# Kernel tuning notes

Hardware: AMD Instinct MI355X
Metric: run time of the kernel (lower is better)

The kernel has to match this reference:

```python
import jax, jax.numpy as jnp
import numpy as np

N_NODES = 50000
N_EDGES = 800000
IN_F = 256
HEADS = 4
C = 32  # out_features // heads = 128 // 4
OUT_F = HEADS * C
NEG_SLOPE = 0.2
BN_EPS = 1e-5


def setup_inputs() -> dict:
    key = jax.random.key(0)
    ks = jax.random.split(key, 6)
    x = jax.random.normal(ks[0], (N_NODES, IN_F), dtype=jnp.float32)
    edge_index = jax.random.randint(ks[1], (2, N_EDGES), 0, N_NODES, dtype=jnp.int64)
    W = jax.random.normal(ks[2], (IN_F, OUT_F), dtype=jnp.float32) * 0.05
    att_src = jax.random.normal(ks[3], (HEADS, C), dtype=jnp.float32) * 0.05
    att_dst = jax.random.normal(ks[4], (HEADS, C), dtype=jnp.float32) * 0.05
    bias = jnp.zeros((OUT_F,), dtype=jnp.float32)
    gamma = jnp.ones((OUT_F,), dtype=jnp.float32)
    beta = jnp.zeros((OUT_F,), dtype=jnp.float32)
    return {"x": x, "edge_index": edge_index, "W": W, "att_src": att_src,
            "att_dst": att_dst, "bias": bias, "gamma": gamma, "beta": beta}


def reference(x, edge_index, W, att_src, att_dst, bias, gamma, beta):
    N = x.shape[0]
    # PyG GATConv adds self-loops by default
    loops = jnp.arange(N, dtype=edge_index.dtype)
    src = jnp.concatenate([edge_index[0], loops])  # [E+N]
    dst = jnp.concatenate([edge_index[1], loops])  # [E+N]

    h = (x @ W).reshape(N, HEADS, C)               # [N, H, C]
    a_src = jnp.sum(h * att_src, axis=-1)          # [N, H]
    a_dst = jnp.sum(h * att_dst, axis=-1)          # [N, H]

    e = a_src[src] + a_dst[dst]                    # [E', H]
    e = jax.nn.leaky_relu(e, NEG_SLOPE)
    # segment softmax over destination neighborhoods (self-loops ensure no empty segments)
    e_max = jax.ops.segment_max(e, dst, num_segments=N)
    e = jnp.exp(e - e_max[dst])
    denom = jax.ops.segment_sum(e, dst, num_segments=N)
    alpha = e / (denom[dst] + 1e-16)               # [E', H]

    msg = h[src] * alpha[:, :, None]               # [E', H, C]
    out = jax.ops.segment_sum(msg, dst, num_segments=N).reshape(N, OUT_F) + bias

    # BatchNorm1d in training mode (batch statistics, biased variance)
    mean = jnp.mean(out, axis=0)
    var = jnp.var(out, axis=0)
    out = (out - mean) * jax.lax.rsqrt(var + BN_EPS) * gamma + beta
    # ELU; dropout is identity in eval / deterministic reference
    return jax.nn.elu(out)
```

## Files before the change

kernel.cpp:

```cpp
#include <hip/hip_runtime.h>
#include <hip/hip_fp16.h>
#include <math.h>

#define NN 50000
#define EE 800000
#define EP (EE + NN)
#define INF_ 256
#define OF 128
#define NEG_SLOPE 0.2f
#define BN_EPS 1e-5f
#define NB 196
#define NWIN 8
#define DPW 6250
#define NCH 32
#define QPC 6250

typedef _Float16 half8 __attribute__((ext_vector_type(8)));
typedef float floatx4 __attribute__((ext_vector_type(4)));
typedef int intx4 __attribute__((ext_vector_type(4)));

__device__ __forceinline__ float lrelu_exp(float v) {
    v = v > 0.f ? v : NEG_SLOPE * v;
    return expf(v);
}

__global__ __launch_bounds__(256) void k_wprep(const float* __restrict__ W, _Float16* __restrict__ wfrag,
                                               float* __restrict__ fsum)
{
    int idx = blockIdx.x * 256 + threadIdx.x;
    if (idx < 256) fsum[idx] = 0.f;
    int j   = idx & 7;
    int l   = (idx >> 3) & 63;
    int t   = (idx >> 9) & 7;
    int ksg = idx >> 12;
    int k   = ksg * 32 + ((l >> 4) << 3) + j;
    int col = t * 16 + (l & 15);
    wfrag[idx] = (_Float16)W[k * OF + col];
}

__global__ __launch_bounds__(256) void k_gemm(
    const float* __restrict__ x, const _Float16* __restrict__ wfrag,
    const float* __restrict__ att_s, const float* __restrict__ att_d,
    _Float16* __restrict__ h, float* __restrict__ a_src, float* __restrict__ a_dst)
{
    __shared__ __align__(16) _Float16 smem[8192];
    _Float16* xh = smem;

    const int tid  = threadIdx.x;
    const int l    = tid & 63;
    const int w    = tid >> 6;
    const int row0 = blockIdx.x * 64;
    const int lrow = l & 15;
    const int lk8  = (l >> 4) << 3;

    floatx4 acc[8];
    #pragma unroll
    for (int t = 0; t < 8; ++t) acc[t] = (floatx4){0.f, 0.f, 0.f, 0.f};

    for (int kc = 0; kc < 4; ++kc) {
        __syncthreads();
        #pragma unroll
        for (int it = 0; it < 4; ++it) {
            int i  = tid + (it << 8);
            int r  = i >> 4;
            int c4 = (i & 15) << 2;
            int rr = row0 + r; if (rr >= NN) rr = NN - 1;
            float4 v = *(const float4*)&x[rr * INF_ + (kc << 6) + c4];
            _Float16* p = &xh[r * 72 + c4];
            p[0] = (_Float16)v.x; p[1] = (_Float16)v.y;
            p[2] = (_Float16)v.z; p[3] = (_Float16)v.w;
        }
        __syncthreads();
        #pragma unroll
        for (int ks = 0; ks < 2; ++ks) {
            int ksg = kc * 2 + ks;
            half8 a = *(half8*)&xh[(w * 16 + lrow) * 72 + (ks << 5) + lk8];
            const _Float16* wf = &wfrag[(ksg << 12) + (l << 3)];
            #pragma unroll
            for (int t = 0; t < 8; ++t) {
                half8 b = *(const half8*)&wf[t << 9];
                acc[t] = __builtin_amdgcn_mfma_f32_16x16x32_f16(a, b, acc[t], 0, 0, 0);
            }
        }
    }

    float as_c[8], ad_c[8];
    #pragma unroll
    for (int t = 0; t < 8; ++t) { as_c[t] = att_s[t * 16 + lrow]; ad_c[t] = att_d[t * 16 + lrow]; }
    float my_s = 0.f, my_d = 0.f;
    #pragma unroll
    for (int hh = 0; hh < 4; ++hh) {
        #pragma unroll
        for (int reg = 0; reg < 4; ++reg) {
            float ps = acc[2*hh][reg] * as_c[2*hh] + acc[2*hh+1][reg] * as_c[2*hh+1];
            float pd = acc[2*hh][reg] * ad_c[2*hh] + acc[2*hh+1][reg] * ad_c[2*hh+1];
            ps += __shfl_xor(ps, 1); ps += __shfl_xor(ps, 2); ps += __shfl_xor(ps, 4); ps += __shfl_xor(ps, 8);
            pd += __shfl_xor(pd, 1); pd += __shfl_xor(pd, 2); pd += __shfl_xor(pd, 4); pd += __shfl_xor(pd, 8);
            if (lrow == hh * 4 + reg) { my_s = ps; my_d = pd; }
        }
    }
    {
        int myreg = lrow & 3, myhh = lrow >> 2;
        int myrow = row0 + w * 16 + ((l >> 4) << 2) + myreg;
        if (myrow < NN) { a_src[myrow * 4 + myhh] = my_s; a_dst[myrow * 4 + myhh] = my_d; }
    }

    __syncthreads();
    _Float16* ldso = smem + w * 2048;
    #pragma unroll
    for (int t = 0; t < 8; ++t)
        #pragma unroll
        for (int reg = 0; reg < 4; ++reg)
            ldso[(((l >> 4) << 2) + reg) * 128 + t * 16 + lrow] = (_Float16)acc[t][reg];
    __syncthreads();
    {
        _Float16* gdst = h + (size_t)(row0 + w * 16) * OF;
        #pragma unroll
        for (int q = 0; q < 4; ++q) {
            int off = (q << 9) + (l << 3);
            *(half8*)&gdst[off] = *(half8*)&ldso[off];
        }
    }
}

__global__ __launch_bounds__(1024) void k_winhist(const int* __restrict__ ei, int* __restrict__ counts2)
{
    __shared__ int hist[DPW];
    const int w   = blockIdx.x & 7;
    const int c   = blockIdx.x >> 3;
    const int dlo = w * DPW;
    for (int i = threadIdx.x; i < DPW; i += 1024) hist[i] = 0;
    __syncthreads();
    const int q0 = c * QPC;
    for (int q = q0 + threadIdx.x; q < q0 + QPC; q += 1024) {
        intx4 d4 = __builtin_nontemporal_load(((const intx4*)(ei + EE)) + q);
        int dj[4] = {d4.x, d4.y, d4.z, d4.w};
        #pragma unroll
        for (int j = 0; j < 4; ++j) {
            unsigned d = (unsigned)(dj[j] - dlo);
            if (d < DPW) atomicAdd(&hist[d], 1);
        }
    }
    __syncthreads();
    int* dst = counts2 + c * NN + dlo;
    for (int i = threadIdx.x; i < DPW; i += 1024) dst[i] = hist[i];
}

__global__ __launch_bounds__(256) void k_blocksum(const int* __restrict__ counts2, int* __restrict__ partials)
{
    int i = blockIdx.x * 256 + threadIdx.x;
    int v = 0;
    if (i < NN) {
        v = 1;
        #pragma unroll 8
        for (int c = 0; c < NCH; ++c) v += counts2[c * NN + i];
    }
    v += __shfl_xor(v, 1);  v += __shfl_xor(v, 2);  v += __shfl_xor(v, 4);
    v += __shfl_xor(v, 8);  v += __shfl_xor(v, 16); v += __shfl_xor(v, 32);
    __shared__ int wsum[4];
    if ((threadIdx.x & 63) == 0) wsum[threadIdx.x >> 6] = v;
    __syncthreads();
    if (threadIdx.x == 0) partials[blockIdx.x] = wsum[0] + wsum[1] + wsum[2] + wsum[3];
}

__global__ __launch_bounds__(256) void k_scanpart(int* __restrict__ partials)
{
    __shared__ int sm[256];
    int t = threadIdx.x;
    int v = (t < NB) ? partials[t] : 0;
    sm[t] = v;
    __syncthreads();
    for (int off = 1; off < 256; off <<= 1) {
        int u = (t >= off) ? sm[t - off] : 0;
        __syncthreads();
        sm[t] += u;
        __syncthreads();
    }
    if (t < NB) partials[t] = sm[t] - v;
}

__global__ __launch_bounds__(256) void k_writerows(
    const int* __restrict__ counts2, const int* __restrict__ partials,
    int* __restrict__ row_start, int* __restrict__ csr_src, int* __restrict__ base)
{
    __shared__ int sm[256];
    int t = threadIdx.x;
    int i = blockIdx.x * 256 + t;
    int v = 0;
    if (i < NN) {
        v = 1;
        #pragma unroll 8
        for (int c = 0; c < NCH; ++c) v += counts2[c * NN + i];
    }
    sm[t] = v;
    __syncthreads();
    for (int off = 1; off < 256; off <<= 1) {
        int u = (t >= off) ? sm[t - off] : 0;
        __syncthreads();
        sm[t] += u;
        __syncthreads();
    }
    int excl = partials[blockIdx.x] + sm[t] - v;
    if (i < NN) {
        row_start[i] = excl;
        csr_src[excl] = i;
        int p = excl + 1;
        #pragma unroll 8
        for (int c = 0; c < NCH; ++c) { base[c * NN + i] = p; p += counts2[c * NN + i]; }
    }
    if (i == NN) row_start[NN] = excl;
}

__global__ __launch_bounds__(1024) void k_winfill(
    const int* __restrict__ ei, const int* __restrict__ base, int* __restrict__ csr_src)
{
    __shared__ int pos[DPW];
    const int w   = blockIdx.x & 7;
    const int c   = blockIdx.x >> 3;
    const int dlo = w * DPW;
    for (int i = threadIdx.x; i < DPW; i += 1024) pos[i] = base[c * NN + dlo + i];
    __syncthreads();
    const int q0 = c * QPC;
    for (int q = q0 + threadIdx.x; q < q0 + QPC; q += 1024) {
        intx4 d4 = __builtin_nontemporal_load(((const intx4*)(ei + EE)) + q);
        int idx0 = q << 2;
        int dj[4] = {d4.x, d4.y, d4.z, d4.w};
        #pragma unroll
        for (int j = 0; j < 4; ++j) {
            unsigned d = (unsigned)(dj[j] - dlo);
            if (d < DPW) {
                int p = atomicAdd(&pos[d], 1);
                csr_src[p] = ei[idx0 + j];
            }
        }
    }
}

__global__ __launch_bounds__(256) void k_alpha(
    const int* __restrict__ csr_src, const int* __restrict__ row_start,
    const float* __restrict__ a_src, const float* __restrict__ a_dst,
    _Float16* __restrict__ csr_alpha)
{
    int gid = blockIdx.x * 256 + threadIdx.x;
    if (gid >= NN * 4) return;
    int node = gid >> 2;
    int hh   = gid & 3;
    int b = row_start[node];
    int e = row_start[node + 1];
    float ad = a_dst[(node << 2) + hh];
    for (int k = b; k < e; ++k) {
        int s = csr_src[k];
        float xv = lrelu_exp(a_src[(s << 2) + hh] + ad);
        csr_alpha[(k << 2) + hh] = (_Float16)xv;
    }
}

__global__ __launch_bounds__(256) void k_gather(
    const _Float16* __restrict__ h, const int* __restrict__ csr_src,
    const _Float16* __restrict__ csr_alpha, const int* __restrict__ row_start,
    const float* __restrict__ bias, _Float16* __restrict__ outh)
{
    int node = blockIdx.x * 4 + (threadIdx.x >> 6);
    int lane = threadIdx.x & 63;
    int g    = lane >> 4;
    int c    = lane & 15;
    int head = c >> 2;
    int b = row_start[node];
    int e = row_start[node + 1];

    float acc[8] = {};
    float dsum = 0.f;
    for (int k = b; k < e; k += 4) {
        int  kk  = k + g;
        bool act = kk < e;
        int  kc  = act ? kk : b;
        int  s   = csr_src[kc];
        float a  = (float)csr_alpha[(kc << 2) + head];
        if (!act) a = 0.f;
        dsum += a;
        half8 hv = *(const half8*)&h[(size_t)s * OF + (c << 3)];
        #pragma unroll
        for (int j = 0; j < 8; ++j)
            acc[j] = fmaf(a, (float)hv[j], acc[j]);
    }
    #pragma unroll
    for (int j = 0; j < 8; ++j) {
        acc[j] += __shfl_xor(acc[j], 16);
        acc[j] += __shfl_xor(acc[j], 32);
    }
    dsum += __shfl_xor(dsum, 16);
    dsum += __shfl_xor(dsum, 32);
    if (g == 0) {
        float inv = 1.0f / (dsum + 1e-16f);
        float4 b0 = *(const float4*)&bias[c << 3];
        float4 b1 = *(const float4*)&bias[(c << 3) + 4];
        float bj[8] = {b0.x, b0.y, b0.z, b0.w, b1.x, b1.y, b1.z, b1.w};
        half8 o;
        #pragma unroll
        for (int j = 0; j < 8; ++j)
            o[j] = (_Float16)fmaf(acc[j], inv, bj[j]);
        *(half8*)&outh[(size_t)node * OF + (c << 3)] = o;
    }
}

__global__ __launch_bounds__(256) void k_bnred(
    const _Float16* __restrict__ outh, float* __restrict__ fsum, float* __restrict__ fsumsq)
{
    int f = threadIdx.x & 127;
    int r = blockIdx.x * 2 + (threadIdx.x >> 7);
    float s = 0.f, ss = 0.f;
    for (; r < NN; r += gridDim.x * 2) {
        float v = (float)outh[r * OF + f];
        s += v;
        ss = fmaf(v, v, ss);
    }
    atomicAdd(&fsum[f], s);
    atomicAdd(&fsumsq[f], ss);
}

__global__ void k_bnfin(
    const float* __restrict__ fsum, const float* __restrict__ fsumsq,
    const float* __restrict__ gamma, const float* __restrict__ beta,
    float* __restrict__ scale, float* __restrict__ shift)
{
    int f = threadIdx.x;
    float mean = fsum[f] * (1.0f / NN);
    float var  = fsumsq[f] * (1.0f / NN) - mean * mean;
    float sc   = gamma[f] * rsqrtf(var + BN_EPS);
    scale[f] = sc;
    shift[f] = beta[f] - mean * sc;
}

__global__ __launch_bounds__(256) void k_apply(
    const _Float16* __restrict__ outh, const float* __restrict__ scale,
    const float* __restrict__ shift, float* __restrict__ out)
{
    int i    = blockIdx.x * 256 + threadIdx.x;
    int base = i << 3;
    int f    = base & 127;
    half8 v  = *(const half8*)&outh[base];
    float4 sc0 = *(const float4*)&scale[f];
    float4 sc1 = *(const float4*)&scale[f + 4];
    float4 sh0 = *(const float4*)&shift[f];
    float4 sh1 = *(const float4*)&shift[f + 4];
    float scj[8] = {sc0.x, sc0.y, sc0.z, sc0.w, sc1.x, sc1.y, sc1.z, sc1.w};
    float shj[8] = {sh0.x, sh0.y, sh0.z, sh0.w, sh1.x, sh1.y, sh1.z, sh1.w};
    float r[8];
    #pragma unroll
    for (int j = 0; j < 8; ++j) {
        float t = fmaf((float)v[j], scj[j], shj[j]);
        r[j] = t > 0.f ? t : expm1f(t);
    }
    *(float4*)&out[base]     = make_float4(r[0], r[1], r[2], r[3]);
    *(float4*)&out[base + 4] = make_float4(r[4], r[5], r[6], r[7]);
}

extern "C" void kernel_launch(void* const* d_in, const int* in_sizes, int n_in,
                              void* d_out, int out_size, void* d_ws, size_t ws_size,
                              hipStream_t stream)
{
    const float* x     = (const float*)d_in[0];
    const int*   ei    = (const int*)d_in[1];
    const float* W     = (const float*)d_in[2];
    const float* att_s = (const float*)d_in[3];
    const float* att_d = (const float*)d_in[4];
    const float* bias  = (const float*)d_in[5];
    const float* gamma = (const float*)d_in[6];
    const float* beta  = (const float*)d_in[7];
    float* out = (float*)d_out;

    float* ws           = (float*)d_ws;
    _Float16* h         = (_Float16*)ws;
    _Float16* outh      = (_Float16*)(ws + 3210000);
    float* a_src        = ws + 6410000;
    float* a_dst        = a_src + 200000;
    float* wfrag_f      = a_dst + 200000;
    float* csr_alpha_f  = wfrag_f + 20000;
    float* fsum         = csr_alpha_f + 1700000;
    float* fsumsq       = fsum + 128;
    float* scale        = fsumsq + 128;
    float* shift        = scale + 128;
    int* row_start      = (int*)(shift + 128);
    int* csr_src        = row_start + NN + 1;
    int* partials       = csr_src + EP;
    int* counts2        = (int*)csr_alpha_f;
    int* cbase          = (int*)outh;
    _Float16* wfrag     = (_Float16*)wfrag_f;
    _Float16* csr_alpha = (_Float16*)csr_alpha_f;

    k_wprep<<<128, 256, 0, stream>>>(W, wfrag, fsum);
    k_gemm<<<(NN + 63) / 64, 256, 0, stream>>>(x, wfrag, att_s, att_d, h, a_src, a_dst);
    k_winhist<<<NWIN * NCH, 1024, 0, stream>>>(ei, counts2);
    k_blocksum<<<NB, 256, 0, stream>>>(counts2, partials);
    k_scanpart<<<1, 256, 0, stream>>>(partials);
    k_writerows<<<NB, 256, 0, stream>>>(counts2, partials, row_start, csr_src, cbase);
    k_winfill<<<NWIN * NCH, 1024, 0, stream>>>(ei, cbase, csr_src);
    k_alpha<<<(NN * 4 + 255) / 256, 256, 0, stream>>>(csr_src, row_start, a_src, a_dst, csr_alpha);
    k_gather<<<NN / 4, 256, 0, stream>>>(h, csr_src, csr_alpha, row_start, bias, outh);
    k_bnred<<<512, 256, 0, stream>>>(outh, fsum, fsumsq);
    k_bnfin<<<1, 128, 0, stream>>>(fsum, fsumsq, gamma, beta, scale, shift);
    k_apply<<<NN * OF / 8 / 256, 256, 0, stream>>>(outh, scale, shift, out);
}
```

Before: 170.9 us.

## Fuse alpha computation into gather and fold scan/bnfin into consumers

Removes three small kernels. The partial-sum scan is now recomputed redundantly inside each k_writerows block. The edge attention logits are computed on the fly in k_gather instead of being materialised as a separate fp16 csr_alpha array. The BN finalisation is computed per block into shared memory in k_apply. This cuts launch overhead and the write and re-read of the per-edge alpha array. In exchange, each gather lane does redundant exp work (four lanes per head share each value), and every writerows and apply block recomputes small prologues.

```diff
diff --git a/kernel.cpp b/kernel.cpp
--- a/kernel.cpp
+++ b/kernel.cpp
@@ -163,28 +163,25 @@
     if (threadIdx.x == 0) partials[blockIdx.x] = wsum[0] + wsum[1] + wsum[2] + wsum[3];
 }
 
-__global__ __launch_bounds__(256) void k_scanpart(int* __restrict__ partials)
-{
-    __shared__ int sm[256];
-    int t = threadIdx.x;
-    int v = (t < NB) ? partials[t] : 0;
-    sm[t] = v;
-    __syncthreads();
-    for (int off = 1; off < 256; off <<= 1) {
-        int u = (t >= off) ? sm[t - off] : 0;
-        __syncthreads();
-        sm[t] += u;
-        __syncthreads();
-    }
-    if (t < NB) partials[t] = sm[t] - v;
-}
-
 __global__ __launch_bounds__(256) void k_writerows(
     const int* __restrict__ counts2, const int* __restrict__ partials,
     int* __restrict__ row_start, int* __restrict__ csr_src, int* __restrict__ base)
 {
+    __shared__ int smp[256];
     __shared__ int sm[256];
     int t = threadIdx.x;
+
+    int pv = (t < NB) ? partials[t] : 0;
+    smp[t] = pv;
+    __syncthreads();
+    for (int off = 1; off < 256; off <<= 1) {
+        int u = (t >= off) ? smp[t - off] : 0;
+        __syncthreads();
+        smp[t] += u;
+        __syncthreads();
+    }
+    int blockoff = (blockIdx.x > 0) ? smp[blockIdx.x - 1] : 0;
+
     int i = blockIdx.x * 256 + t;
     int v = 0;
     if (i < NN) {
@@ -200,7 +197,7 @@
         sm[t] += u;
         __syncthreads();
     }
-    int excl = partials[blockIdx.x] + sm[t] - v;
+    int excl = blockoff + sm[t] - v;
     if (i < NN) {
         row_start[i] = excl;
         csr_src[excl] = i;
@@ -236,29 +233,11 @@
     }
 }
 
-__global__ __launch_bounds__(256) void k_alpha(
-    const int* __restrict__ csr_src, const int* __restrict__ row_start,
-    const float* __restrict__ a_src, const float* __restrict__ a_dst,
-    _Float16* __restrict__ csr_alpha)
-{
-    int gid = blockIdx.x * 256 + threadIdx.x;
-    if (gid >= NN * 4) return;
-    int node = gid >> 2;
-    int hh   = gid & 3;
-    int b = row_start[node];
-    int e = row_start[node + 1];
-    float ad = a_dst[(node << 2) + hh];
-    for (int k = b; k < e; ++k) {
-        int s = csr_src[k];
-        float xv = lrelu_exp(a_src[(s << 2) + hh] + ad);
-        csr_alpha[(k << 2) + hh] = (_Float16)xv;
-    }
-}
-
 __global__ __launch_bounds__(256) void k_gather(
     const _Float16* __restrict__ h, const int* __restrict__ csr_src,
-    const _Float16* __restrict__ csr_alpha, const int* __restrict__ row_start,
-    const float* __restrict__ bias, _Float16* __restrict__ outh)
+    const int* __restrict__ row_start, const float* __restrict__ a_src,
+    const float* __restrict__ a_dst, const float* __restrict__ bias,
+    _Float16* __restrict__ outh)
 {
     int node = blockIdx.x * 4 + (threadIdx.x >> 6);
     int lane = threadIdx.x & 63;
@@ -267,6 +246,7 @@
     int head = c >> 2;
     int b = row_start[node];
     int e = row_start[node + 1];
+    float ad = a_dst[(node << 2) + head];
 
     float acc[8] = {};
     float dsum = 0.f;
@@ -275,7 +255,7 @@
         bool act = kk < e;
         int  kc  = act ? kk : b;
         int  s   = csr_src[kc];
-        float a  = (float)csr_alpha[(kc << 2) + head];
+        float a  = lrelu_exp(a_src[(s << 2) + head] + ad);
         if (!act) a = 0.f;
         dsum += a;
         half8 hv = *(const half8*)&h[(size_t)s * OF + (c << 3)];
@@ -318,37 +298,29 @@
     atomicAdd(&fsumsq[f], ss);
 }
 
-__global__ void k_bnfin(
-    const float* __restrict__ fsum, const float* __restrict__ fsumsq,
-    const float* __restrict__ gamma, const float* __restrict__ beta,
-    float* __restrict__ scale, float* __restrict__ shift)
-{
-    int f = threadIdx.x;
-    float mean = fsum[f] * (1.0f / NN);
-    float var  = fsumsq[f] * (1.0f / NN) - mean * mean;
-    float sc   = gamma[f] * rsqrtf(var + BN_EPS);
-    scale[f] = sc;
-    shift[f] = beta[f] - mean * sc;
-}
-
 __global__ __launch_bounds__(256) void k_apply(
-    const _Float16* __restrict__ outh, const float* __restrict__ scale,
-    const float* __restrict__ shift, float* __restrict__ out)
-{
+    const _Float16* __restrict__ outh, const float* __restrict__ fsum,
+    const float* __restrict__ fsumsq, const float* __restrict__ gamma,
+    const float* __restrict__ beta, float* __restrict__ out)
+{
+    __shared__ float ssc[128], ssh[128];
+    if (threadIdx.x < 128) {
+        int f = threadIdx.x;
+        float mean = fsum[f] * (1.0f / NN);
+        float var  = fsumsq[f] * (1.0f / NN) - mean * mean;
+        float sc   = gamma[f] * rsqrtf(var + BN_EPS);
+        ssc[f] = sc;
+        ssh[f] = beta[f] - mean * sc;
+    }
+    __syncthreads();
     int i    = blockIdx.x * 256 + threadIdx.x;
     int base = i << 3;
     int f    = base & 127;
     half8 v  = *(const half8*)&outh[base];
-    float4 sc0 = *(const float4*)&scale[f];
-    float4 sc1 = *(const float4*)&scale[f + 4];
-    float4 sh0 = *(const float4*)&shift[f];
-    float4 sh1 = *(const float4*)&shift[f + 4];
-    float scj[8] = {sc0.x, sc0.y, sc0.z, sc0.w, sc1.x, sc1.y, sc1.z, sc1.w};
-    float shj[8] = {sh0.x, sh0.y, sh0.z, sh0.w, sh1.x, sh1.y, sh1.z, sh1.w};
     float r[8];
     #pragma unroll
     for (int j = 0; j < 8; ++j) {
-        float t = fmaf((float)v[j], scj[j], shj[j]);
+        float t = fmaf((float)v[j], ssc[f + j], ssh[f + j]);
         r[j] = t > 0.f ? t : expm1f(t);
     }
     *(float4*)&out[base]     = make_float4(r[0], r[1], r[2], r[3]);
@@ -375,29 +347,23 @@
     float* a_src        = ws + 6410000;
     float* a_dst        = a_src + 200000;
     float* wfrag_f      = a_dst + 200000;
-    float* csr_alpha_f  = wfrag_f + 20000;
-    float* fsum         = csr_alpha_f + 1700000;
+    float* scratch_f    = wfrag_f + 20000;
+    float* fsum         = scratch_f + 1700000;
     float* fsumsq       = fsum + 128;
-    float* scale        = fsumsq + 128;
-    float* shift        = scale + 128;
-    int* row_start      = (int*)(shift + 128);
+    int* row_start      = (int*)(fsumsq + 128);
     int* csr_src        = row_start + NN + 1;
     int* partials       = csr_src + EP;
-    int* counts2        = (int*)csr_alpha_f;
+    int* counts2        = (int*)scratch_f;
     int* cbase          = (int*)outh;
     _Float16* wfrag     = (_Float16*)wfrag_f;
-    _Float16* csr_alpha = (_Float16*)csr_alpha_f;
 
     k_wprep<<<128, 256, 0, stream>>>(W, wfrag, fsum);
     k_gemm<<<(NN + 63) / 64, 256, 0, stream>>>(x, wfrag, att_s, att_d, h, a_src, a_dst);
     k_winhist<<<NWIN * NCH, 1024, 0, stream>>>(ei, counts2);
     k_blocksum<<<NB, 256, 0, stream>>>(counts2, partials);
-    k_scanpart<<<1, 256, 0, stream>>>(partials);
     k_writerows<<<NB, 256, 0, stream>>>(counts2, partials, row_start, csr_src, cbase);
     k_winfill<<<NWIN * NCH, 1024, 0, stream>>>(ei, cbase, csr_src);
-    k_alpha<<<(NN * 4 + 255) / 256, 256, 0, stream>>>(csr_src, row_start, a_src, a_dst, csr_alpha);
-    k_gather<<<NN / 4, 256, 0, stream>>>(h, csr_src, csr_alpha, row_start, bias, outh);
+    k_gather<<<NN / 4, 256, 0, stream>>>(h, csr_src, row_start, a_src, a_dst, bias, outh);
     k_bnred<<<512, 256, 0, stream>>>(outh, fsum, fsumsq);
-    k_bnfin<<<1, 128, 0, stream>>>(fsum, fsumsq, gamma, beta, scale, shift);
-    k_apply<<<NN * OF / 8 / 256, 256, 0, stream>>>(outh, scale, shift, out);
-}
+    k_apply<<<NN * OF / 8 / 256, 256, 0, stream>>>(outh, fsum, fsumsq, gamma, beta, out);
+}
```

Measured after the change: 155.8 us. -8.8%, faster.
